# Optimization experiments

Measured on AMD Instinct MI355X. Metric: run time of the kernel, lower is better.

Reference implementation:

```python
import jax, jax.numpy as jnp
import numpy as np

HEADS = 16
EPS = 1e-5

def layer_norm(x, gamma, beta):
    mu = jnp.mean(x, axis=-1, keepdims=True)
    var = jnp.mean(jnp.square(x - mu), axis=-1, keepdims=True)
    return (x - mu) * jax.lax.rsqrt(var + EPS) * gamma + beta

def setup_inputs() -> dict:
    key = jax.random.key(0)
    ks = jax.random.split(key, 5)
    d = 384
    hd = HEADS * d  # 6144
    scale = 1.0 / np.sqrt(d)
    return {
        "x": jax.random.normal(ks[0], (4, 14, 14, d), dtype=jnp.float32),
        "Wq": jax.random.normal(ks[1], (d, hd), dtype=jnp.float32) * scale,
        "Wk": jax.random.normal(ks[2], (d, hd), dtype=jnp.float32) * scale,
        "Wv": jax.random.normal(ks[3], (d, hd), dtype=jnp.float32) * scale,
        "Wout": jax.random.normal(ks[4], (hd, d), dtype=jnp.float32) * (1.0 / np.sqrt(hd)),
        "gamma": jnp.ones((d,), dtype=jnp.float32),
        "beta": jnp.zeros((d,), dtype=jnp.float32),
    }

def reference(x, Wq, Wk, Wv, Wout, gamma, beta):
    bs, h, w, d = x.shape
    n = h * w
    sqrt_norm = jnp.asarray(np.sqrt(d), dtype=x.dtype)
    # pre_norm = True: normalize input, residual uses normalized x (as in torch code)
    xn = layer_norm(x, gamma, beta)
    xf = xn.reshape(bs, n, d)
    # (bs, n, heads, d) -> (bs, d, n, heads): model_dim acts as heads, num_heads as head_dim
    def proj(W):
        return (xf @ W).reshape(bs, n, HEADS, d).transpose(0, 3, 1, 2)
    q, k, v = proj(Wq), proj(Wk), proj(Wv)
    scores = jnp.einsum('bdih,bdjh->bdij', q, k) / sqrt_norm  # (bs, d, n, n)
    probs = jax.nn.softmax(scores, axis=-1)  # dropout p=0 (eval)
    out = jnp.einsum('bdij,bdjh->bdih', probs, v)  # (bs, d, n, heads)
    out = out.transpose(0, 2, 3, 1).reshape(bs, h, w, HEADS * d)
    out = out @ Wout + xn
    return out, probs
```

## Files before the change

kernel.cpp:

```cpp
#include <hip/hip_runtime.h>
#include <math.h>

#define BS 4
#define NTOK 196
#define DCH 384
#define HD 6144
#define ROWS (BS*NTOK)
#define MPAD 896
#define SCALE 0.05103103630798287f

typedef unsigned short u16;
typedef __attribute__((ext_vector_type(8))) short bf8v;
typedef __attribute__((ext_vector_type(4))) float f4v;
typedef __attribute__((ext_vector_type(16))) float f16v;
typedef __attribute__((ext_vector_type(8))) unsigned short u16x8;
typedef __attribute__((ext_vector_type(4))) unsigned short u16x4;
typedef __attribute__((ext_vector_type(2))) unsigned int u32x2;

static __device__ __forceinline__ float b2f(u16 u) {
    unsigned int x = ((unsigned int)u) << 16;
    float f; __builtin_memcpy(&f, &x, 4); return f;
}
static __device__ __forceinline__ u16 f2b(float f) {
    unsigned int x; __builtin_memcpy(&x, &f, 4);
    unsigned int r = x + 0x7FFF + ((x >> 16) & 1);
    return (u16)(r >> 16);
}
static __device__ __forceinline__ unsigned int pack2(float lo, float hi) {
    unsigned int r;
    asm("v_cvt_pk_bf16_f32 %0, %1, %2" : "=v"(r) : "v"(lo), "v"(hi));
    return r;
}
static __device__ __forceinline__ float blo(unsigned int u) {
    unsigned int x = u << 16; float f; __builtin_memcpy(&f, &x, 4); return f;
}
static __device__ __forceinline__ float bhi(unsigned int u) {
    unsigned int x = u & 0xffff0000u; float f; __builtin_memcpy(&f, &x, 4); return f;
}

__global__ __launch_bounds__(128) void ln_kernel(
    const float* __restrict__ x, const float* __restrict__ gamma,
    const float* __restrict__ beta, float* __restrict__ xn, u16* __restrict__ xnb)
{
    int row = blockIdx.x;
    int t = threadIdx.x;
    if (row >= ROWS) {
        xnb[(size_t)row*DCH + t] = 0;
        xnb[(size_t)row*DCH + t + 128] = 0;
        xnb[(size_t)row*DCH + t + 256] = 0;
        return;
    }
    const float* xr = x + (size_t)row * DCH;
    float v0 = xr[t], v1 = xr[t + 128], v2 = xr[t + 256];
    float s  = v0 + v1 + v2;
    float ss = v0*v0 + v1*v1 + v2*v2;
    #pragma unroll
    for (int off = 1; off < 64; off <<= 1) {
        s  += __shfl_xor(s,  off);
        ss += __shfl_xor(ss, off);
    }
    __shared__ float red[4];
    int wv = t >> 6;
    if ((t & 63) == 0) { red[wv*2] = s; red[wv*2+1] = ss; }
    __syncthreads();
    float S = red[0] + red[2], SS = red[1] + red[3];
    float mu  = S * (1.0f / DCH);
    float var = SS * (1.0f / DCH) - mu * mu;
    float inv = rsqrtf(var + 1e-5f);
    float* xo = xn + (size_t)row * DCH;
    u16*   xb = xnb + (size_t)row * DCH;
    float r0 = (v0 - mu) * inv * gamma[t]       + beta[t];
    float r1 = (v1 - mu) * inv * gamma[t + 128] + beta[t + 128];
    float r2 = (v2 - mu) * inv * gamma[t + 256] + beta[t + 256];
    xo[t] = r0; xo[t+128] = r1; xo[t+256] = r2;
    xb[t] = f2b(r0); xb[t+128] = f2b(r1); xb[t+256] = f2b(r2);
}

__global__ __launch_bounds__(256) void convert_w_kernel(
    const float* __restrict__ Wq, const float* __restrict__ Wk, const float* __restrict__ Wv,
    u16* __restrict__ Wqb, u16* __restrict__ Wkb, u16* __restrict__ Wvb)
{
    const float* W = (blockIdx.z == 0) ? Wq : (blockIdx.z == 1) ? Wk : Wv;
    u16* Wb        = (blockIdx.z == 0) ? Wqb : (blockIdx.z == 1) ? Wkb : Wvb;
    __shared__ u16 tbuf[32][33];
    int tid = threadIdx.x;
    int k0 = blockIdx.y * 32, n0 = blockIdx.x * 32;
    #pragma unroll
    for (int it = 0; it < 4; it++) {
        int e = it*256 + tid; int kk = e >> 5, nn = e & 31;
        tbuf[kk][nn] = f2b(W[(size_t)(k0+kk)*HD + n0 + nn]);
    }
    __syncthreads();
    #pragma unroll
    for (int it = 0; it < 4; it++) {
        int e = it*256 + tid; int nn = e >> 5, kk = e & 31;
        int n_orig = n0 + nn;
        int np = (blockIdx.z == 2) ? n_orig : ((n_orig % DCH)*16 + n_orig / DCH);
        Wb[(size_t)np*DCH + k0 + kk] = tbuf[kk][nn];
    }
}

__global__ __launch_bounds__(256) void convert_wout_kernel(
    const float* __restrict__ Wout, u16* __restrict__ Woutb)
{
    __shared__ u16 tbuf[128][65];
    int tid = threadIdx.x;
    int dc0 = blockIdx.x * 8;
    int n0  = blockIdx.y * 64;
    #pragma unroll
    for (int it = 0; it < 32; it++) {
        int e = it*256 + tid; int r = e >> 6, c = e & 63;
        int h = r >> 3, d = r & 7;
        tbuf[r][c] = f2b(Wout[(size_t)(h*DCH + dc0 + d)*DCH + n0 + c]);
    }
    __syncthreads();
    #pragma unroll
    for (int it = 0; it < 32; it++) {
        int e = it*256 + tid; int n = e >> 7, kk = e & 127;
        Woutb[(size_t)(n0+n)*HD + dc0*16 + kk] = tbuf[(kk & 15)*8 + (kk >> 4)][n];
    }
}

__global__ __launch_bounds__(256) void gemm_qkv(
    const u16* __restrict__ xnb,
    const u16* __restrict__ Wqb, const u16* __restrict__ Wkb, const u16* __restrict__ Wvb,
    u16* __restrict__ qt, u16* __restrict__ kt, u16* __restrict__ vt)
{
    const u16* Wb = (blockIdx.z == 0) ? Wqb : (blockIdx.z == 1) ? Wkb : Wvb;
    u16* C        = (blockIdx.z == 0) ? qt : (blockIdx.z == 1) ? kt : vt;
    __shared__ u16 As[128*64];
    __shared__ u16 Bs[128*64];
    int tid = threadIdx.x, lane = tid & 63, wv = tid >> 6;
    int wm = wv >> 1, wn = wv & 1;
    int row0 = blockIdx.y * 128, col0 = blockIdx.x * 128;
    f4v acc[4][4] = {};
    int rsub = tid >> 3;
    int g8 = tid & 7;
    int g8s = g8 ^ (rsub & 7);

    for (int k0 = 0; k0 < 384; k0 += 64) {
        u16x8 ra[4], rb[4];
        #pragma unroll
        for (int c = 0; c < 4; c++) {
            int row = c*32 + rsub;
            ra[c] = *(const u16x8*)(xnb + (size_t)(row0+row)*DCH + k0 + g8*8);
            rb[c] = *(const u16x8*)(Wb  + (size_t)(col0+row)*DCH + k0 + g8*8);
        }
        __syncthreads();
        #pragma unroll
        for (int c = 0; c < 4; c++) {
            int row = c*32 + rsub;
            *(u16x8*)&As[row*64 + g8s*8] = ra[c];
            *(u16x8*)&Bs[row*64 + g8s*8] = rb[c];
        }
        __syncthreads();
        #pragma unroll
        for (int ks = 0; ks < 2; ks++) {
            int gr = (ks*4 + (lane >> 4)) ^ (lane & 7);
            bf8v af[4], bf[4];
            #pragma unroll
            for (int m = 0; m < 4; m++)
                af[m] = *(const bf8v*)&As[(wm*64 + m*16 + (lane & 15))*64 + gr*8];
            #pragma unroll
            for (int n = 0; n < 4; n++)
                bf[n] = *(const bf8v*)&Bs[(wn*64 + n*16 + (lane & 15))*64 + gr*8];
            #pragma unroll
            for (int m = 0; m < 4; m++)
                #pragma unroll
                for (int n = 0; n < 4; n++)
                    acc[m][n] = __builtin_amdgcn_mfma_f32_16x16x32_bf16(af[m], bf[n], acc[m][n], 0, 0, 0);
        }
    }
    int cb = lane & 15, rg = lane >> 4;
    #pragma unroll
    for (int m = 0; m < 4; m++) {
        int r0 = row0 + wm*64 + m*16 + rg*4;
        if (r0 >= ROWS) continue;
        int b = r0 / NTOK, i = r0 - b*NTOK;
        #pragma unroll
        for (int n = 0; n < 4; n++) {
            int nb = col0 + wn*64 + n*16;
            if (blockIdx.z == 2) {
                int ncol = nb + cb;
                int h = ncol / DCH, dc = ncol - h*DCH;
                size_t addr = ((size_t)((b*DCH + dc)*16 + h))*NTOK + i;
                u16x4 o = {f2b(acc[m][n][0]), f2b(acc[m][n][1]), f2b(acc[m][n][2]), f2b(acc[m][n][3])};
                *(u16x4*)(C + addr) = o;
            } else {
                int dc = nb >> 4;
                size_t a2 = ((size_t)(b*DCH + dc))*(NTOK*16) + (size_t)i*16 + cb;
                C[a2]      = f2b(acc[m][n][0]);
                C[a2 + 16] = f2b(acc[m][n][1]);
                C[a2 + 32] = f2b(acc[m][n][2]);
                C[a2 + 48] = f2b(acc[m][n][3]);
            }
        }
    }
}

__global__ __launch_bounds__(256) void attn_kernel(
    const u16* __restrict__ qt, const u16* __restrict__ kt, const u16* __restrict__ vt,
    float* __restrict__ probs, u16* __restrict__ ot2)
{
    __shared__ u16 Klds[NTOK*16];
    __shared__ u16 Vlds[NTOK*16 + 16];
    __shared__ u16 Plds[4][2048];
    __shared__ float invs[4][32];
    int bd = blockIdx.x;
    int b = bd / DCH, dc = bd - b*DCH;
    int tid = threadIdx.x;
    int wv = tid >> 6;
    int it = blockIdx.y*4 + wv;
    int lane = tid & 63;
    int l31 = lane & 31, hi = lane >> 5;
    const u16* qb = qt + (size_t)bd * (NTOK*16);
    const u16* kb = kt + (size_t)bd * (NTOK*16);
    const u16* vb = vt + (size_t)bd * (NTOK*16);

    for (int e8 = tid; e8 < (NTOK*16)/8; e8 += 256) {
        *(u16x8*)&Klds[e8*8] = *(const u16x8*)(kb + e8*8);
        *(u16x8*)&Vlds[e8*8] = *(const u16x8*)(vb + e8*8);
    }
    __syncthreads();
    if (it >= 7) return;
    u16* Pw = Plds[wv];

    int iq = it*32 + l31;
    int iqc = iq < NTOK ? iq : NTOK-1;
    bf8v qf = *(const bf8v*)(qb + iqc*16 + hi*8);

    unsigned int P[6][8];
    float et[4];
    float s0 = 0.f, s1 = 0.f, s2 = 0.f, s3 = 0.f;

    #pragma unroll
    for (int jt = 0; jt < 7; jt++) {
        int j = jt*32 + l31;
        int jc = j < NTOK ? j : NTOK-1;
        bf8v kf = *(const bf8v*)&Klds[jc*16 + hi*8];
        f16v z = {};
        f16v Sv = __builtin_amdgcn_mfma_f32_32x32x16_bf16(kf, qf, z, 0, 0, 0);
        if (jt < 6) {
            float e[16];
            #pragma unroll
            for (int r = 0; r < 16; r++) e[r] = __expf(Sv[r] * SCALE);
            #pragma unroll
            for (int r = 0; r < 16; r += 4) {
                s0 += e[r]; s1 += e[r+1]; s2 += e[r+2]; s3 += e[r+3];
            }
            #pragma unroll
            for (int g = 0; g < 4; g++) {
                P[jt][2*g]   = pack2(e[4*g],   e[4*g+1]);
                P[jt][2*g+1] = pack2(e[4*g+2], e[4*g+3]);
            }
        } else {
            #pragma unroll
            for (int r = 0; r < 4; r++)
                et[r] = (hi == 0) ? __expf(Sv[r] * SCALE) : 0.f;
            s0 += et[0]; s1 += et[1]; s2 += et[2]; s3 += et[3];
        }
    }
    float Sig = (s0 + s1) + (s2 + s3);
    Sig += __shfl_xor(Sig, 32);
    float inv = 1.0f / Sig;
    if (hi == 0) invs[wv][l31] = inv;

    float* prow_base = probs + (size_t)bd * NTOK * NTOK;
    f16v O = {};
    int row_lo = lane >> 4;
    int scol   = lane & 15;

    #pragma unroll
    for (int jtp = 0; jtp < 3; jtp++) {
        #pragma unroll
        for (int jtl = 0; jtl < 2; jtl++) {
            int jt = jtp*2 + jtl;
            #pragma unroll
            for (int g = 0; g < 4; g++) {
                int cs  = jtl*8 + 2*g + hi;
                int csw = cs ^ ((l31 & 7) << 1);
                u32x2 w2 = {P[jt][2*g], P[jt][2*g+1]};
                *(u32x2*)&Pw[l31*64 + csw*4] = w2;
            }
        }
        #pragma unroll
        for (int rr = 0; rr < 8; rr++) {
            int row = rr*4 + row_lo;
            float rinv = invs[wv][row];
            int csw = scol ^ ((row & 7) << 1);
            u32x2 pv = *(const u32x2*)&Pw[row*64 + csw*4];
            int gi = it*32 + row;
            if (gi < NTOK) {
                f4v o = {blo(pv.x)*rinv, bhi(pv.x)*rinv, blo(pv.y)*rinv, bhi(pv.y)*rinv};
                *(f4v*)(prow_base + (size_t)gi*NTOK + jtp*64 + scol*4) = o;
            }
        }
        #pragma unroll
        for (int jtl = 0; jtl < 2; jtl++) {
            #pragma unroll
            for (int u = 0; u < 2; u++) {
                int m  = jtl*4 + u*2 + hi;
                int mw = m ^ (l31 & 7);
                bf8v pf = *(const bf8v*)&Pw[l31*64 + mw*8];
                int j0 = jtp*64 + jtl*32 + u*16 + hi*8;
                int off = (l31 & 15)*NTOK + j0;
                u16x4 vlo = *(const u16x4*)&Vlds[off];
                u16x4 vh4 = *(const u16x4*)&Vlds[off + 4];
                u16 varr[8];
                #pragma unroll
                for (int e = 0; e < 4; e++) { varr[e] = vlo[e]; varr[4+e] = vh4[e]; }
                bf8v vf; __builtin_memcpy(&vf, varr, 16);
                O = __builtin_amdgcn_mfma_f32_32x32x16_bf16(pf, vf, O, 0, 0, 0);
            }
        }
    }

    if (hi == 0 && iq < NTOK) {
        f4v o = {et[0]*inv, et[1]*inv, et[2]*inv, et[3]*inv};
        *(f4v*)(prow_base + (size_t)iq*NTOK + 192) = o;
    }
    {
        u16 arr[8];
        #pragma unroll
        for (int e = 0; e < 4; e++) {
            arr[e]   = (hi == 0) ? f2b(et[e]) : (u16)0;
            arr[4+e] = 0;
        }
        bf8v pf; __builtin_memcpy(&pf, arr, 16);
        int j0 = 192 + hi*8;
        int off = (l31 & 15)*NTOK + j0;
        u16x4 vlo = *(const u16x4*)&Vlds[off];
        u16x4 vh4 = *(const u16x4*)&Vlds[off + 4];
        u16 varr[8];
        #pragma unroll
        for (int e = 0; e < 4; e++) { varr[e] = vlo[e]; varr[4+e] = vh4[e]; }
        bf8v vf; __builtin_memcpy(&vf, varr, 16);
        O = __builtin_amdgcn_mfma_f32_32x32x16_bf16(pf, vf, O, 0, 0, 0);
    }

    if (l31 < 16) {
        #pragma unroll
        for (int r = 0; r < 16; r++) {
            int il = (r & 3) + 8*(r >> 2) + 4*hi;
            int i = it*32 + il;
            if (i < NTOK) {
                float iv = invs[wv][il];
                ot2[((size_t)(b*NTOK + i))*HD + dc*16 + l31] = f2b(O[r] * iv);
            }
        }
    }
}

__global__ __launch_bounds__(256) void gemm_wout(
    const u16* __restrict__ A, const u16* __restrict__ Bw, float* __restrict__ partial)
{
    __shared__ u16 As[128*64];
    __shared__ u16 Bs[128*64];
    int tid = threadIdx.x, lane = tid & 63, wv = tid >> 6;
    int wm = wv >> 1, wn = wv & 1;
    int row0 = blockIdx.y * 128, col0 = blockIdx.x * 128;
    int kbase = blockIdx.z * 256;
    f4v acc[4][4] = {};
    int rsub = tid >> 3;
    int g8 = tid & 7;
    int g8s = g8 ^ (rsub & 7);

    for (int k0 = kbase; k0 < kbase + 256; k0 += 64) {
        u16x8 ra[4], rb[4];
        #pragma unroll
        for (int c = 0; c < 4; c++) {
            int row = c*32 + rsub;
            int arow = row0 + row; if (arow > ROWS-1) arow = ROWS-1;
            ra[c] = *(const u16x8*)(A  + (size_t)arow*HD + k0 + g8*8);
            rb[c] = *(const u16x8*)(Bw + (size_t)(col0+row)*HD + k0 + g8*8);
        }
        __syncthreads();
        #pragma unroll
        for (int c = 0; c < 4; c++) {
            int row = c*32 + rsub;
            *(u16x8*)&As[row*64 + g8s*8] = ra[c];
            *(u16x8*)&Bs[row*64 + g8s*8] = rb[c];
        }
        __syncthreads();
        #pragma unroll
        for (int ks = 0; ks < 2; ks++) {
            int gr = (ks*4 + (lane >> 4)) ^ (lane & 7);
            bf8v af[4], bf[4];
            #pragma unroll
            for (int m = 0; m < 4; m++)
                af[m] = *(const bf8v*)&As[(wm*64 + m*16 + (lane & 15))*64 + gr*8];
            #pragma unroll
            for (int n = 0; n < 4; n++)
                bf[n] = *(const bf8v*)&Bs[(wn*64 + n*16 + (lane & 15))*64 + gr*8];
            #pragma unroll
            for (int m = 0; m < 4; m++)
                #pragma unroll
                for (int n = 0; n < 4; n++)
                    acc[m][n] = __builtin_amdgcn_mfma_f32_16x16x32_bf16(af[m], bf[n], acc[m][n], 0, 0, 0);
        }
    }
    float* Pp = partial + (size_t)blockIdx.z * ROWS * DCH;
    int cb = lane & 15, rg = lane >> 4;
    #pragma unroll
    for (int m = 0; m < 4; m++) {
        int r0 = row0 + wm*64 + m*16 + rg*4;
        #pragma unroll
        for (int n = 0; n < 4; n++) {
            int ncol = col0 + wn*64 + n*16 + cb;
            #pragma unroll
            for (int j = 0; j < 4; j++) {
                int r = r0 + j;
                if (r < ROWS) Pp[(size_t)r*DCH + ncol] = acc[m][n][j];
            }
        }
    }
}

__global__ __launch_bounds__(256) void reduce_out_kernel(
    const float* __restrict__ partial, const float* __restrict__ xn, float* __restrict__ out)
{
    int e = blockIdx.x * 256 + threadIdx.x;
    if (e < ROWS * DCH) {
        float s = xn[e];
        #pragma unroll
        for (int c = 0; c < 24; c++)
            s += partial[(size_t)c * ROWS * DCH + e];
        out[e] = s;
    }
}

extern "C" void kernel_launch(void* const* d_in, const int* in_sizes, int n_in,
                              void* d_out, int out_size, void* d_ws, size_t ws_size,
                              hipStream_t stream) {
    (void)in_sizes; (void)n_in; (void)out_size; (void)ws_size;
    const float* x     = (const float*)d_in[0];
    const float* Wq    = (const float*)d_in[1];
    const float* Wk    = (const float*)d_in[2];
    const float* Wv    = (const float*)d_in[3];
    const float* Wout  = (const float*)d_in[4];
    const float* gamma = (const float*)d_in[5];
    const float* beta  = (const float*)d_in[6];

    float* out   = (float*)d_out;
    float* probs = out + (size_t)ROWS * DCH;

    char* w = (char*)d_ws;
    float* xn  = (float*)w;  w += (size_t)ROWS*DCH*4;
    u16* xnb   = (u16*)w;    w += (size_t)MPAD*DCH*2;
    u16* Wqb   = (u16*)w;    w += (size_t)HD*DCH*2;
    u16* Wkb   = (u16*)w;    w += (size_t)HD*DCH*2;
    u16* Wvb   = (u16*)w;    w += (size_t)HD*DCH*2;
    u16* Woutb = (u16*)w;    w += (size_t)DCH*HD*2;
    u16* qt    = (u16*)w;    w += (size_t)ROWS*HD*2;
    u16* kt    = (u16*)w;    w += (size_t)ROWS*HD*2;
    u16* vt    = (u16*)w;    w += (size_t)ROWS*HD*2;
    u16* ot2   = (u16*)w;    w += (size_t)ROWS*HD*2;
    float* partial = (float*)qt;

    hipLaunchKernelGGL(ln_kernel, dim3(MPAD), dim3(128), 0, stream, x, gamma, beta, xn, xnb);
    hipLaunchKernelGGL(convert_w_kernel, dim3(192, 12, 3), dim3(256), 0, stream,
                       Wq, Wk, Wv, Wqb, Wkb, Wvb);
    hipLaunchKernelGGL(convert_wout_kernel, dim3(48, 6), dim3(256), 0, stream, Wout, Woutb);
    hipLaunchKernelGGL(gemm_qkv, dim3(48, 7, 3), dim3(256), 0, stream,
                       xnb, Wqb, Wkb, Wvb, qt, kt, vt);
    hipLaunchKernelGGL(attn_kernel, dim3(BS * DCH, 2), dim3(256), 0, stream,
                       qt, kt, vt, probs, ot2);
    hipLaunchKernelGGL(gemm_wout, dim3(3, 7, 24), dim3(256), 0, stream, ot2, Woutb, partial);
    hipLaunchKernelGGL(reduce_out_kernel, dim3((ROWS * DCH + 255) / 256), dim3(256), 0, stream,
                       partial, xn, out);
}
```

Baseline: 133.8 us.

## Merge weight conversions, use 7-wave attention blocks, drop fp32 normalized copy

Combines the QKV and Wout weight conversion kernels into a single launch with a flattened block index, which removes one kernel launch. The attention kernel now uses one 448-thread block per (batch, channel) with 7 waves, so K/V are loaded into LDS once instead of twice and no waves sit idle. The fp32 copy of the layer-normed input is dropped and the residual is read back from the bf16 copy, which saves a write and a read but lowers the precision of the residual term. The merged conversion kernel reserves LDS for both tile buffers in every block, which could reduce occupancy.

```diff
diff --git a/kernel.cpp b/kernel.cpp
--- a/kernel.cpp
+++ b/kernel.cpp
@@ -40,7 +40,7 @@
 
 __global__ __launch_bounds__(128) void ln_kernel(
     const float* __restrict__ x, const float* __restrict__ gamma,
-    const float* __restrict__ beta, float* __restrict__ xn, u16* __restrict__ xnb)
+    const float* __restrict__ beta, u16* __restrict__ xnb)
 {
     int row = blockIdx.x;
     int t = threadIdx.x;
@@ -67,57 +67,56 @@
     float mu  = S * (1.0f / DCH);
     float var = SS * (1.0f / DCH) - mu * mu;
     float inv = rsqrtf(var + 1e-5f);
-    float* xo = xn + (size_t)row * DCH;
-    u16*   xb = xnb + (size_t)row * DCH;
-    float r0 = (v0 - mu) * inv * gamma[t]       + beta[t];
-    float r1 = (v1 - mu) * inv * gamma[t + 128] + beta[t + 128];
-    float r2 = (v2 - mu) * inv * gamma[t + 256] + beta[t + 256];
-    xo[t] = r0; xo[t+128] = r1; xo[t+256] = r2;
-    xb[t] = f2b(r0); xb[t+128] = f2b(r1); xb[t+256] = f2b(r2);
-}
-
-__global__ __launch_bounds__(256) void convert_w_kernel(
+    u16* xb = xnb + (size_t)row * DCH;
+    xb[t]       = f2b((v0 - mu) * inv * gamma[t]       + beta[t]);
+    xb[t + 128] = f2b((v1 - mu) * inv * gamma[t + 128] + beta[t + 128]);
+    xb[t + 256] = f2b((v2 - mu) * inv * gamma[t + 256] + beta[t + 256]);
+}
+
+__global__ __launch_bounds__(256) void convert_all_kernel(
     const float* __restrict__ Wq, const float* __restrict__ Wk, const float* __restrict__ Wv,
-    u16* __restrict__ Wqb, u16* __restrict__ Wkb, u16* __restrict__ Wvb)
-{
-    const float* W = (blockIdx.z == 0) ? Wq : (blockIdx.z == 1) ? Wk : Wv;
-    u16* Wb        = (blockIdx.z == 0) ? Wqb : (blockIdx.z == 1) ? Wkb : Wvb;
+    const float* __restrict__ Wout,
+    u16* __restrict__ Wqb, u16* __restrict__ Wkb, u16* __restrict__ Wvb,
+    u16* __restrict__ Woutb)
+{
     __shared__ u16 tbuf[32][33];
+    __shared__ u16 tbuf2[128][65];
+    int bid = blockIdx.x;
     int tid = threadIdx.x;
-    int k0 = blockIdx.y * 32, n0 = blockIdx.x * 32;
-    #pragma unroll
-    for (int it = 0; it < 4; it++) {
-        int e = it*256 + tid; int kk = e >> 5, nn = e & 31;
-        tbuf[kk][nn] = f2b(W[(size_t)(k0+kk)*HD + n0 + nn]);
-    }
-    __syncthreads();
-    #pragma unroll
-    for (int it = 0; it < 4; it++) {
-        int e = it*256 + tid; int nn = e >> 5, kk = e & 31;
-        int n_orig = n0 + nn;
-        int np = (blockIdx.z == 2) ? n_orig : ((n_orig % DCH)*16 + n_orig / DCH);
-        Wb[(size_t)np*DCH + k0 + kk] = tbuf[kk][nn];
-    }
-}
-
-__global__ __launch_bounds__(256) void convert_wout_kernel(
-    const float* __restrict__ Wout, u16* __restrict__ Woutb)
-{
-    __shared__ u16 tbuf[128][65];
-    int tid = threadIdx.x;
-    int dc0 = blockIdx.x * 8;
-    int n0  = blockIdx.y * 64;
-    #pragma unroll
-    for (int it = 0; it < 32; it++) {
-        int e = it*256 + tid; int r = e >> 6, c = e & 63;
-        int h = r >> 3, d = r & 7;
-        tbuf[r][c] = f2b(Wout[(size_t)(h*DCH + dc0 + d)*DCH + n0 + c]);
-    }
-    __syncthreads();
-    #pragma unroll
-    for (int it = 0; it < 32; it++) {
-        int e = it*256 + tid; int n = e >> 7, kk = e & 127;
-        Woutb[(size_t)(n0+n)*HD + dc0*16 + kk] = tbuf[(kk & 15)*8 + (kk >> 4)][n];
+    if (bid < 6912) {
+        int z = bid / 2304, rem = bid - z*2304;
+        int k0 = (rem / 192) * 32, n0 = (rem % 192) * 32;
+        const float* W = (z == 0) ? Wq : (z == 1) ? Wk : Wv;
+        u16* Wb        = (z == 0) ? Wqb : (z == 1) ? Wkb : Wvb;
+        #pragma unroll
+        for (int it = 0; it < 4; it++) {
+            int e = it*256 + tid; int kk = e >> 5, nn = e & 31;
+            tbuf[kk][nn] = f2b(W[(size_t)(k0+kk)*HD + n0 + nn]);
+        }
+        __syncthreads();
+        #pragma unroll
+        for (int it = 0; it < 4; it++) {
+            int e = it*256 + tid; int nn = e >> 5, kk = e & 31;
+            int n_orig = n0 + nn;
+            int np = (z == 2) ? n_orig : ((n_orig % DCH)*16 + n_orig / DCH);
+            Wb[(size_t)np*DCH + k0 + kk] = tbuf[kk][nn];
+        }
+    } else {
+        int b2 = bid - 6912;
+        int dc0 = (b2 % 48) * 8;
+        int n0  = (b2 / 48) * 64;
+        #pragma unroll
+        for (int it = 0; it < 32; it++) {
+            int e = it*256 + tid; int r = e >> 6, c = e & 63;
+            int h = r >> 3, d = r & 7;
+            tbuf2[r][c] = f2b(Wout[(size_t)(h*DCH + dc0 + d)*DCH + n0 + c]);
+        }
+        __syncthreads();
+        #pragma unroll
+        for (int it = 0; it < 32; it++) {
+            int e = it*256 + tid; int n = e >> 7, kk = e & 127;
+            Woutb[(size_t)(n0+n)*HD + dc0*16 + kk] = tbuf2[(kk & 15)*8 + (kk >> 4)][n];
+        }
     }
 }
 
@@ -198,31 +197,30 @@
     }
 }
 
-__global__ __launch_bounds__(256) void attn_kernel(
+__global__ __launch_bounds__(448) void attn_kernel(
     const u16* __restrict__ qt, const u16* __restrict__ kt, const u16* __restrict__ vt,
     float* __restrict__ probs, u16* __restrict__ ot2)
 {
     __shared__ u16 Klds[NTOK*16];
     __shared__ u16 Vlds[NTOK*16 + 16];
-    __shared__ u16 Plds[4][2048];
-    __shared__ float invs[4][32];
+    __shared__ u16 Plds[7][2048];
+    __shared__ float invs[7][32];
     int bd = blockIdx.x;
     int b = bd / DCH, dc = bd - b*DCH;
     int tid = threadIdx.x;
     int wv = tid >> 6;
-    int it = blockIdx.y*4 + wv;
+    int it = wv;
     int lane = tid & 63;
     int l31 = lane & 31, hi = lane >> 5;
     const u16* qb = qt + (size_t)bd * (NTOK*16);
     const u16* kb = kt + (size_t)bd * (NTOK*16);
     const u16* vb = vt + (size_t)bd * (NTOK*16);
 
-    for (int e8 = tid; e8 < (NTOK*16)/8; e8 += 256) {
+    for (int e8 = tid; e8 < (NTOK*16)/8; e8 += 448) {
         *(u16x8*)&Klds[e8*8] = *(const u16x8*)(kb + e8*8);
         *(u16x8*)&Vlds[e8*8] = *(const u16x8*)(vb + e8*8);
     }
     __syncthreads();
-    if (it >= 7) return;
     u16* Pw = Plds[wv];
 
     int iq = it*32 + l31;
@@ -417,11 +415,11 @@
 }
 
 __global__ __launch_bounds__(256) void reduce_out_kernel(
-    const float* __restrict__ partial, const float* __restrict__ xn, float* __restrict__ out)
+    const float* __restrict__ partial, const u16* __restrict__ xnb, float* __restrict__ out)
 {
     int e = blockIdx.x * 256 + threadIdx.x;
     if (e < ROWS * DCH) {
-        float s = xn[e];
+        float s = b2f(xnb[e]);
         #pragma unroll
         for (int c = 0; c < 24; c++)
             s += partial[(size_t)c * ROWS * DCH + e];
@@ -445,7 +443,6 @@
     float* probs = out + (size_t)ROWS * DCH;
 
     char* w = (char*)d_ws;
-    float* xn  = (float*)w;  w += (size_t)ROWS*DCH*4;
     u16* xnb   = (u16*)w;    w += (size_t)MPAD*DCH*2;
     u16* Wqb   = (u16*)w;    w += (size_t)HD*DCH*2;
     u16* Wkb   = (u16*)w;    w += (size_t)HD*DCH*2;
@@ -457,15 +454,14 @@
     u16* ot2   = (u16*)w;    w += (size_t)ROWS*HD*2;
     float* partial = (float*)qt;
 
-    hipLaunchKernelGGL(ln_kernel, dim3(MPAD), dim3(128), 0, stream, x, gamma, beta, xn, xnb);
-    hipLaunchKernelGGL(convert_w_kernel, dim3(192, 12, 3), dim3(256), 0, stream,
-                       Wq, Wk, Wv, Wqb, Wkb, Wvb);
-    hipLaunchKernelGGL(convert_wout_kernel, dim3(48, 6), dim3(256), 0, stream, Wout, Woutb);
+    hipLaunchKernelGGL(ln_kernel, dim3(MPAD), dim3(128), 0, stream, x, gamma, beta, xnb);
+    hipLaunchKernelGGL(convert_all_kernel, dim3(7200), dim3(256), 0, stream,
+                       Wq, Wk, Wv, Wout, Wqb, Wkb, Wvb, Woutb);
     hipLaunchKernelGGL(gemm_qkv, dim3(48, 7, 3), dim3(256), 0, stream,
                        xnb, Wqb, Wkb, Wvb, qt, kt, vt);
-    hipLaunchKernelGGL(attn_kernel, dim3(BS * DCH, 2), dim3(256), 0, stream,
+    hipLaunchKernelGGL(attn_kernel, dim3(BS * DCH), dim3(448), 0, stream,
                        qt, kt, vt, probs, ot2);
     hipLaunchKernelGGL(gemm_wout, dim3(3, 7, 24), dim3(256), 0, stream, ot2, Woutb, partial);
     hipLaunchKernelGGL(reduce_out_kernel, dim3((ROWS * DCH + 255) / 256), dim3(256), 0, stream,
-                       partial, xn, out);
-}
+                       partial, xnb, out);
+}
```

Result: faster. 128.8 us, median of 3 (-3.7%).
